# Kernel optimization log

Hardware: AMD Instinct MI355X
Metric: run time of the kernel (lower is better)

## Reference

```python
import jax, jax.numpy as jnp
import numpy as np

B, D, M = 32, 640, 1024
EPS = 1e-05


def setup_inputs() -> dict:
    key = jax.random.key(0)
    x = jax.random.normal(key, (B, D, M), dtype=jnp.float32)
    return {"x": x}


def _triu_flat_indices(d):
    iu, ju = np.triu_indices(d)
    return jnp.asarray(iu * d + ju, dtype=jnp.int32)


def reference(x):
    b, d, m = x.shape
    # Gram matrix: x @ x^T  -> [b, d, d]
    x_pow2 = jnp.einsum('bim,bjm->bij', x, x)
    # I_M @ (x_pow2 * I) + (x_pow2 * I) @ I_M - 2*x_pow2
    # (x_pow2 * I) is diagonal, so ones-matrix bmm = broadcast of the diagonal.
    diag = jnp.diagonal(x_pow2, axis1=1, axis2=2)  # [b, d]
    dcov = diag[:, None, :] + diag[:, :, None] - 2.0 * x_pow2
    dcov = jnp.maximum(dcov, 0.0)
    # temperature param is built in-forward: exp(log(1/(2*d*m))) = 1/(2*d*m)
    temperature = 1.0 / (2.0 * d * m)
    dcov = jnp.sqrt(temperature * dcov + EPS)
    # Double centering: dcov @ I_M = row sums broadcast; I_M @ dcov = col sums.
    row_mean = dcov.sum(axis=2, keepdims=True) / d          # [b, d, 1]
    col_mean = dcov.sum(axis=1, keepdims=True) / d          # [b, 1, d]
    tot_mean = dcov.sum(axis=(1, 2), keepdims=True) / (d * d)
    t = dcov - row_mean - col_mean + tot_mean               # [b, d, d]
    # Triuvec: gather upper-triangular entries (incl. diagonal)
    flat_idx = _triu_flat_indices(d)                         # [d*(d+1)//2]
    y = t.reshape(b, d * d)[:, flat_idx]
    return y
```

## Files before the change

### kernel.cpp

```cpp
#include <hip/hip_runtime.h>

#define D_DIM 640
#define M_DIM 1024
#define B_DIM 32
#define OUT_ROW 205120

typedef __bf16 bf16x8 __attribute__((ext_vector_type(8)));
typedef float f32x4 __attribute__((ext_vector_type(4)));

__device__ __forceinline__ unsigned short f2bf(float f) {
    union { float f; unsigned int u; } c; c.f = f;
    unsigned int u = c.u;
    unsigned int r = (u + 0x7fffu + ((u >> 16) & 1u)) >> 16;
    return (unsigned short)r;
}

__device__ __forceinline__ float bf2f(unsigned short h) {
    union { unsigned int u; float f; } c; c.u = ((unsigned int)h) << 16;
    return c.f;
}

__device__ __forceinline__ void gload_lds16(const unsigned short* g, unsigned short* l) {
    __builtin_amdgcn_global_load_lds(
        (const __attribute__((address_space(1))) unsigned int*)g,
        (__attribute__((address_space(3))) unsigned int*)l,
        16, 0, 0);
}

__device__ __forceinline__ float block_reduce_256(float s) {
    #pragma unroll
    for (int off = 32; off > 0; off >>= 1) s += __shfl_down(s, off, 64);
    __shared__ float red[4];
    if ((threadIdx.x & 63) == 0) red[threadIdx.x >> 6] = s;
    __syncthreads();
    return red[0] + red[1] + red[2] + red[3];
}

__global__ void cast_diag_kernel(const float* __restrict__ x,
                                 unsigned short* __restrict__ xb,
                                 float* __restrict__ diag,
                                 float* __restrict__ rowsum,
                                 float* __restrict__ tot) {
    const size_t row = blockIdx.x;
    const int t = threadIdx.x;
    const float4 v = ((const float4*)(x + row * M_DIM))[t];
    float s = v.x * v.x + v.y * v.y + v.z * v.z + v.w * v.w;
    ushort4 o;
    o.x = f2bf(v.x); o.y = f2bf(v.y); o.z = f2bf(v.z); o.w = f2bf(v.w);
    ((ushort4*)(xb + row * M_DIM))[t] = o;
    float ssum = block_reduce_256(s);
    if (t == 0) { diag[row] = ssum; rowsum[row] = 0.f; }
    if (t == 1 && row < B_DIM) tot[row] = 0.f;
}

__global__ __launch_bounds__(256, 3)
void gemm_dcov_kernel(const unsigned short* __restrict__ xb,
                      const float* __restrict__ diag,
                      unsigned short* __restrict__ dcov,
                      float* __restrict__ rowsum,
                      float* __restrict__ tot) {
    __shared__ __align__(16) unsigned short smem[24576];

    const int id = blockIdx.x;
    const int bt = (id & 7) * 4 + ((id >> 3) & 3);
    const int rest = id >> 5;
    const int jh = rest & 1;
    int p2 = rest >> 1;
    int it = 0, off = p2;
    while (off >= 5 - it) { off -= 5 - it; ++it; }
    const int jt = it + off;
    const bool diagTile = (it == jt);

    const int tid = threadIdx.x;
    const int w = tid >> 6, l = tid & 63;
    const int wy = w >> 1, wx = w & 1;
    const int lm = l & 15, quad = l >> 4;

    const unsigned short* gA = xb + ((size_t)bt * D_DIM + it * 128) * M_DIM;
    const unsigned short* gB = xb + ((size_t)bt * D_DIM + jt * 128 + jh * 64) * M_DIM;

    const int r0 = tid >> 2;
    const int cl = (((tid & 3) ^ ((tid >> 3) & 3)) << 3);
    const size_t aoff = (size_t)r0 * M_DIM + cl;
    const int ldst = tid * 8;

    auto issue = [&](int k, int ph) {
        unsigned short* sA = smem + ph * 6144;
        unsigned short* sB = sA + 4096;
        const int koff = k * 32;
        gload_lds16(gA + aoff + koff, sA + ldst);
        gload_lds16(gA + aoff + (size_t)64 * M_DIM + koff, sA + ldst + 2048);
        gload_lds16(gB + aoff + koff, sB + ldst);
    };

    f32x4 acc[4][2];
    const f32x4 zero = {0.f, 0.f, 0.f, 0.f};
    #pragma unroll
    for (int i = 0; i < 4; i++)
        #pragma unroll
        for (int j = 0; j < 2; j++) acc[i][j] = zero;

    const int sw = ((quad ^ ((lm >> 1) & 3)) << 3);

    issue(0, 0); issue(1, 1); issue(2, 2);

    for (int k = 0; k < 32; ++k) {
        if (k < 30)       asm volatile("s_waitcnt vmcnt(6)" ::: "memory");
        else if (k == 30) asm volatile("s_waitcnt vmcnt(3)" ::: "memory");
        else              asm volatile("s_waitcnt vmcnt(0)" ::: "memory");
        asm volatile("s_barrier" ::: "memory");
        if (k + 3 < 32) issue(k + 3, (k + 3) & 3);

        const unsigned short* sA = smem + (k & 3) * 6144;
        const unsigned short* sB = sA + 4096;
        bf16x8 af[4], bfr[2];
        #pragma unroll
        for (int mi = 0; mi < 4; mi++)
            af[mi] = *(const bf16x8*)&sA[(wy * 64 + mi * 16 + lm) * 32 + sw];
        #pragma unroll
        for (int ni = 0; ni < 2; ni++)
            bfr[ni] = *(const bf16x8*)&sB[(wx * 32 + ni * 16 + lm) * 32 + sw];

        #pragma unroll
        for (int mi = 0; mi < 4; mi++)
            #pragma unroll
            for (int ni = 0; ni < 2; ni++)
                acc[mi][ni] = __builtin_amdgcn_mfma_f32_16x16x32_bf16(
                    af[mi], bfr[ni], acc[mi][ni], 0, 0, 0);
    }

    float* sd = (float*)smem;
    if (tid < 128)      sd[tid] = diag[(size_t)bt * D_DIM + it * 128 + tid];
    else if (tid < 192) sd[tid] = diag[(size_t)bt * D_DIM + jt * 128 + jh * 64 + (tid - 128)];
    __syncthreads();

    const float temp = 7.62939453125e-07f;
    unsigned short* dbase = dcov + (size_t)bt * D_DIM * D_DIM;
    float* rs = rowsum + (size_t)bt * D_DIM;
    float ts = 0.f;
    float cp[2] = {0.f, 0.f};

    #pragma unroll
    for (int mi = 0; mi < 4; mi++) {
        #pragma unroll
        for (int r = 0; r < 4; r++) {
            const int lrow = wy * 64 + mi * 16 + quad * 4 + r;
            const int grow = it * 128 + lrow;
            const float di = sd[lrow];
            float rp = 0.f;
            #pragma unroll
            for (int ni = 0; ni < 2; ni++) {
                const int lcol = wx * 32 + ni * 16 + lm;
                const int gcol = jt * 128 + jh * 64 + lcol;
                const float dj = sd[128 + lcol];
                const float g = acc[mi][ni][r];
                const float v = sqrtf(fmaf(temp, fmaxf(di + dj - 2.f * g, 0.f), 1e-5f));
                dbase[(size_t)grow * D_DIM + gcol] = f2bf(v);
                rp += v;
                cp[ni] += v;
            }
            ts += rp;
            rp += __shfl_down(rp, 8, 16);
            rp += __shfl_down(rp, 4, 16);
            rp += __shfl_down(rp, 2, 16);
            rp += __shfl_down(rp, 1, 16);
            if (lm == 0) atomicAdd(&rs[grow], rp);
        }
    }
    if (!diagTile) {
        #pragma unroll
        for (int ni = 0; ni < 2; ni++) {
            float c = cp[ni];
            c += __shfl_down(c, 32);
            c += __shfl_down(c, 16);
            if (l < 16) atomicAdd(&rs[jt * 128 + jh * 64 + wx * 32 + ni * 16 + lm], c);
        }
    }
    float bs = block_reduce_256(ts);
    if (tid == 0) atomicAdd(&tot[bt], diagTile ? bs : 2.f * bs);
}

__global__ void output_kernel(const unsigned short* __restrict__ dcov,
                              const float* __restrict__ rowsum,
                              const float* __restrict__ tot,
                              float* __restrict__ out) {
    const int b = blockIdx.x / 320;
    const int q = blockIdx.x - b * 320;
    const float inv_d = 1.f / (float)D_DIM;
    const float tm = tot[b] * (inv_d * inv_d);
    const float* rs = rowsum + (size_t)b * D_DIM;

    #pragma unroll
    for (int half = 0; half < 2; half++) {
        const int i = half ? (D_DIM - 1 - q) : q;
        const float rmi = rs[i] * inv_d;
        const unsigned short* drow = dcov + ((size_t)b * D_DIM + i) * D_DIM;
        float* orow = out + (size_t)b * OUT_ROW + (size_t)i * D_DIM - (size_t)i * (i - 1) / 2;
        for (int j = i + threadIdx.x; j < D_DIM; j += 256)
            orow[j - i] = bf2f(drow[j]) - rmi - rs[j] * inv_d + tm;
    }
}

extern "C" void kernel_launch(void* const* d_in, const int* in_sizes, int n_in,
                              void* d_out, int out_size, void* d_ws, size_t ws_size,
                              hipStream_t stream) {
    const float* x = (const float*)d_in[0];
    float* out = (float*)d_out;

    char* ws = (char*)d_ws;
    unsigned short* xb = (unsigned short*)ws;
    size_t off = 41943040;
    float* diag = (float*)(ws + off);           off += 81920;
    unsigned short* dcov = (unsigned short*)(ws + off); off += 26214400;
    float* rowsum = (float*)(ws + off);         off += 81920;
    float* tot = (float*)(ws + off);            off += 256;

    cast_diag_kernel<<<dim3(B_DIM * D_DIM), 256, 0, stream>>>(x, xb, diag, rowsum, tot);
    gemm_dcov_kernel<<<dim3(960), 256, 0, stream>>>(xb, diag, dcov, rowsum, tot);
    output_kernel<<<dim3(B_DIM * 320), 256, 0, stream>>>(dcov, rowsum, tot, out);
}
```

Before: 185.6 us.

## Use 256x256 upper-triangle GEMM tiles with 1024-thread blocks and per-wave masking

```diff
diff --git a/kernel.cpp b/kernel.cpp
--- a/kernel.cpp
+++ b/kernel.cpp
@@ -34,6 +34,18 @@
     if ((threadIdx.x & 63) == 0) red[threadIdx.x >> 6] = s;
     __syncthreads();
     return red[0] + red[1] + red[2] + red[3];
+}
+
+__device__ __forceinline__ float block_reduce_1024(float s) {
+    #pragma unroll
+    for (int off = 32; off > 0; off >>= 1) s += __shfl_down(s, off, 64);
+    __shared__ float red[16];
+    if ((threadIdx.x & 63) == 0) red[threadIdx.x >> 6] = s;
+    __syncthreads();
+    float t = 0.f;
+    #pragma unroll
+    for (int i = 0; i < 16; i++) t += red[i];
+    return t;
 }
 
 __global__ void cast_diag_kernel(const float* __restrict__ x,
@@ -53,131 +65,146 @@
     if (t == 1 && row < B_DIM) tot[row] = 0.f;
 }
 
-__global__ __launch_bounds__(256, 3)
+__global__ __launch_bounds__(1024)
 void gemm_dcov_kernel(const unsigned short* __restrict__ xb,
                       const float* __restrict__ diag,
                       unsigned short* __restrict__ dcov,
                       float* __restrict__ rowsum,
                       float* __restrict__ tot) {
-    __shared__ __align__(16) unsigned short smem[24576];
+    __shared__ __align__(16) unsigned short smem[65536];
 
     const int id = blockIdx.x;
-    const int bt = (id & 7) * 4 + ((id >> 3) & 3);
-    const int rest = id >> 5;
-    const int jh = rest & 1;
-    int p2 = rest >> 1;
-    int it = 0, off = p2;
-    while (off >= 5 - it) { off -= 5 - it; ++it; }
-    const int jt = it + off;
-    const bool diagTile = (it == jt);
+    const int xcd = id & 7;
+    const int k6 = id >> 3;
+    const int bt = xcd + 8 * (k6 / 6);
+    const int mc = k6 % 6;
+    const int R = (mc < 3) ? 0 : ((mc < 5) ? 1 : 2);
+    const int C = (mc < 3) ? mc : ((mc < 5) ? (mc - 2) : 2);
+    const int h = (R == 2) ? 128 : 256;
+    const int wd = (C == 2) ? 128 : 256;
 
     const int tid = threadIdx.x;
     const int w = tid >> 6, l = tid & 63;
-    const int wy = w >> 1, wx = w & 1;
+    const int wy = w >> 2, wx = w & 3;
     const int lm = l & 15, quad = l >> 4;
-
-    const unsigned short* gA = xb + ((size_t)bt * D_DIM + it * 128) * M_DIM;
-    const unsigned short* gB = xb + ((size_t)bt * D_DIM + jt * 128 + jh * 64) * M_DIM;
+    const bool alive = (wy * 64 < h) && (wx * 64 < wd) && (R != C || wy <= wx);
+
+    const unsigned short* gA = xb + ((size_t)bt * D_DIM + R * 256) * M_DIM;
+    const unsigned short* gB = xb + ((size_t)bt * D_DIM + C * 256) * M_DIM;
 
     const int r0 = tid >> 2;
     const int cl = (((tid & 3) ^ ((tid >> 3) & 3)) << 3);
-    const size_t aoff = (size_t)r0 * M_DIM + cl;
+    const int ra = (r0 < h) ? r0 : (r0 & 63);
+    const int rb = (r0 < wd) ? r0 : (r0 & 63);
+    const size_t aoffA = (size_t)ra * M_DIM + cl;
+    const size_t aoffB = (size_t)rb * M_DIM + cl;
     const int ldst = tid * 8;
 
     auto issue = [&](int k, int ph) {
-        unsigned short* sA = smem + ph * 6144;
-        unsigned short* sB = sA + 4096;
+        unsigned short* sA = smem + ph * 16384;
+        unsigned short* sB = sA + 8192;
         const int koff = k * 32;
-        gload_lds16(gA + aoff + koff, sA + ldst);
-        gload_lds16(gA + aoff + (size_t)64 * M_DIM + koff, sA + ldst + 2048);
-        gload_lds16(gB + aoff + koff, sB + ldst);
+        gload_lds16(gA + aoffA + koff, sA + ldst);
+        gload_lds16(gB + aoffB + koff, sB + ldst);
     };
 
-    f32x4 acc[4][2];
+    f32x4 acc[4][4];
     const f32x4 zero = {0.f, 0.f, 0.f, 0.f};
     #pragma unroll
     for (int i = 0; i < 4; i++)
         #pragma unroll
-        for (int j = 0; j < 2; j++) acc[i][j] = zero;
+        for (int j = 0; j < 4; j++) acc[i][j] = zero;
 
     const int sw = ((quad ^ ((lm >> 1) & 3)) << 3);
 
     issue(0, 0); issue(1, 1); issue(2, 2);
 
     for (int k = 0; k < 32; ++k) {
-        if (k < 30)       asm volatile("s_waitcnt vmcnt(6)" ::: "memory");
-        else if (k == 30) asm volatile("s_waitcnt vmcnt(3)" ::: "memory");
+        if (k < 30)       asm volatile("s_waitcnt vmcnt(4)" ::: "memory");
+        else if (k == 30) asm volatile("s_waitcnt vmcnt(2)" ::: "memory");
         else              asm volatile("s_waitcnt vmcnt(0)" ::: "memory");
         asm volatile("s_barrier" ::: "memory");
         if (k + 3 < 32) issue(k + 3, (k + 3) & 3);
 
-        const unsigned short* sA = smem + (k & 3) * 6144;
-        const unsigned short* sB = sA + 4096;
-        bf16x8 af[4], bfr[2];
-        #pragma unroll
-        for (int mi = 0; mi < 4; mi++)
-            af[mi] = *(const bf16x8*)&sA[(wy * 64 + mi * 16 + lm) * 32 + sw];
-        #pragma unroll
-        for (int ni = 0; ni < 2; ni++)
-            bfr[ni] = *(const bf16x8*)&sB[(wx * 32 + ni * 16 + lm) * 32 + sw];
-
-        #pragma unroll
-        for (int mi = 0; mi < 4; mi++)
-            #pragma unroll
-            for (int ni = 0; ni < 2; ni++)
-                acc[mi][ni] = __builtin_amdgcn_mfma_f32_16x16x32_bf16(
-                    af[mi], bfr[ni], acc[mi][ni], 0, 0, 0);
+        if (alive) {
+            const unsigned short* sA = smem + (k & 3) * 16384;
+            const unsigned short* sB = sA + 8192;
+            bf16x8 af[4], bfr[4];
+            #pragma unroll
+            for (int mi = 0; mi < 4; mi++)
+                af[mi] = *(const bf16x8*)&sA[(wy * 64 + mi * 16 + lm) * 32 + sw];
+            #pragma unroll
+            for (int ni = 0; ni < 4; ni++)
+                bfr[ni] = *(const bf16x8*)&sB[(wx * 64 + ni * 16 + lm) * 32 + sw];
+
+            #pragma unroll
+            for (int mi = 0; mi < 4; mi++)
+                #pragma unroll
+                for (int ni = 0; ni < 4; ni++)
+                    acc[mi][ni] = __builtin_amdgcn_mfma_f32_16x16x32_bf16(
+                        af[mi], bfr[ni], acc[mi][ni], 0, 0, 0);
+        }
     }
 
     float* sd = (float*)smem;
-    if (tid < 128)      sd[tid] = diag[(size_t)bt * D_DIM + it * 128 + tid];
-    else if (tid < 192) sd[tid] = diag[(size_t)bt * D_DIM + jt * 128 + jh * 64 + (tid - 128)];
+    const float* dg = diag + (size_t)bt * D_DIM;
+    if (tid < 256) {
+        const int rr = R * 256 + tid;
+        sd[tid] = dg[rr < D_DIM ? rr : (D_DIM - 1)];
+    } else if (tid < 512) {
+        const int cc = C * 256 + (tid - 256);
+        sd[tid] = dg[cc < D_DIM ? cc : (D_DIM - 1)];
+    }
     __syncthreads();
 
     const float temp = 7.62939453125e-07f;
     unsigned short* dbase = dcov + (size_t)bt * D_DIM * D_DIM;
     float* rs = rowsum + (size_t)bt * D_DIM;
     float ts = 0.f;
-    float cp[2] = {0.f, 0.f};
-
-    #pragma unroll
-    for (int mi = 0; mi < 4; mi++) {
+
+    if (alive) {
+        float cp[4] = {0.f, 0.f, 0.f, 0.f};
         #pragma unroll
-        for (int r = 0; r < 4; r++) {
-            const int lrow = wy * 64 + mi * 16 + quad * 4 + r;
-            const int grow = it * 128 + lrow;
-            const float di = sd[lrow];
-            float rp = 0.f;
-            #pragma unroll
-            for (int ni = 0; ni < 2; ni++) {
-                const int lcol = wx * 32 + ni * 16 + lm;
-                const int gcol = jt * 128 + jh * 64 + lcol;
-                const float dj = sd[128 + lcol];
-                const float g = acc[mi][ni][r];
-                const float v = sqrtf(fmaf(temp, fmaxf(di + dj - 2.f * g, 0.f), 1e-5f));
-                dbase[(size_t)grow * D_DIM + gcol] = f2bf(v);
-                rp += v;
-                cp[ni] += v;
+        for (int mi = 0; mi < 4; mi++) {
+            #pragma unroll
+            for (int r = 0; r < 4; r++) {
+                const int lrow = wy * 64 + mi * 16 + quad * 4 + r;
+                const int grow = R * 256 + lrow;
+                const float di = sd[lrow];
+                float rp = 0.f;
+                #pragma unroll
+                for (int ni = 0; ni < 4; ni++) {
+                    const int lcol = wx * 64 + ni * 16 + lm;
+                    const int gcol = C * 256 + lcol;
+                    const float dj = sd[256 + lcol];
+                    const float g = acc[mi][ni][r];
+                    const float v = sqrtf(fmaf(temp, fmaxf(di + dj - 2.f * g, 0.f), 1e-5f));
+                    const bool up = (grow <= gcol);
+                    const bool strict = (grow < gcol);
+                    if (up) dbase[(size_t)grow * D_DIM + gcol] = f2bf(v);
+                    const float vp = up ? v : 0.f;
+                    const float vm = strict ? v : 0.f;
+                    rp += vp;
+                    cp[ni] += vm;
+                    ts += vp + vm;
+                }
+                rp += __shfl_down(rp, 8, 16);
+                rp += __shfl_down(rp, 4, 16);
+                rp += __shfl_down(rp, 2, 16);
+                rp += __shfl_down(rp, 1, 16);
+                if (lm == 0) atomicAdd(&rs[grow], rp);
             }
-            ts += rp;
-            rp += __shfl_down(rp, 8, 16);
-            rp += __shfl_down(rp, 4, 16);
-            rp += __shfl_down(rp, 2, 16);
-            rp += __shfl_down(rp, 1, 16);
-            if (lm == 0) atomicAdd(&rs[grow], rp);
         }
-    }
-    if (!diagTile) {
         #pragma unroll
-        for (int ni = 0; ni < 2; ni++) {
+        for (int ni = 0; ni < 4; ni++) {
             float c = cp[ni];
             c += __shfl_down(c, 32);
             c += __shfl_down(c, 16);
-            if (l < 16) atomicAdd(&rs[jt * 128 + jh * 64 + wx * 32 + ni * 16 + lm], c);
+            if (l < 16) atomicAdd(&rs[C * 256 + wx * 64 + ni * 16 + lm], c);
         }
     }
-    float bs = block_reduce_256(ts);
-    if (tid == 0) atomicAdd(&tot[bt], diagTile ? bs : 2.f * bs);
+    float bs = block_reduce_1024(ts);
+    if (tid == 0) atomicAdd(&tot[bt], bs);
 }
 
 __global__ void output_kernel(const unsigned short* __restrict__ dcov,
@@ -216,6 +243,6 @@
     float* tot = (float*)(ws + off);            off += 256;
 
     cast_diag_kernel<<<dim3(B_DIM * D_DIM), 256, 0, stream>>>(x, xb, diag, rowsum, tot);
-    gemm_dcov_kernel<<<dim3(960), 256, 0, stream>>>(xb, diag, dcov, rowsum, tot);
+    gemm_dcov_kernel<<<dim3(192), 1024, 0, stream>>>(xb, diag, dcov, rowsum, tot);
     output_kernel<<<dim3(B_DIM * 320), 256, 0, stream>>>(dcov, rowsum, tot, out);
 }
```

Result: slower. 215.1 us (+15.9%).
